# Performance work log

Measured on AMD Instinct MI355X. Metric: run time of the kernel, lower is better.

The kernel has to match this reference:

```python
import jax, jax.numpy as jnp
import numpy as np

N_TOK = 16384   # total tokens (batch*seq)
H = 2048        # hidden_size
I = 768         # moe_intermediate_size (per-expert MLP width)
TOPK = 8        # num_experts_per_tok


def setup_inputs() -> dict:
    key = jax.random.key(0)
    ks = jax.random.split(key, 7)
    hidden_states = jax.random.normal(ks[0], (N_TOK, H), dtype=jnp.float32)
    # expert_mask[j, k] != 0 means token k selected this expert at top-k slot j
    expert_mask = jax.random.randint(ks[1], (TOPK, N_TOK), 0, 2, dtype=jnp.int32)
    routing_weights = jax.random.uniform(ks[2], (N_TOK, TOPK), dtype=jnp.float32)
    final_hidden_states = jax.random.normal(ks[3], (N_TOK, H), dtype=jnp.float32)
    gate_w = jax.random.normal(ks[4], (I, H), dtype=jnp.float32) * 0.02
    up_w = jax.random.normal(ks[5], (I, H), dtype=jnp.float32) * 0.02
    down_w = jax.random.normal(ks[6], (H, I), dtype=jnp.float32) * 0.02
    return {
        "hidden_states": hidden_states,
        "expert_mask": expert_mask,
        "routing_weights": routing_weights,
        "final_hidden_states": final_hidden_states,
        "gate_w": gate_w,
        "up_w": up_w,
        "down_w": down_w,
    }


def reference(hidden_states, expert_mask, routing_weights, final_hidden_states,
              gate_w, up_w, down_w):
    # forward_expert: gather selected tokens, SwiGLU MLP, scale by routing weight,
    # scatter-add into final_hidden_states. Equivalent jit-friendly form: the
    # combined routing weight per token is w[k] = sum_j mask[j,k]*routing_weights[k,j]
    # (tokens selected multiple times are summed, matching index_add_ semantics),
    # and unselected tokens get w[k]=0 so they contribute nothing.
    g = hidden_states @ gate_w.T                       # [N, I]
    u = hidden_states @ up_w.T                         # [N, I]
    y = (jax.nn.silu(g) * u) @ down_w.T                # [N, H]
    w = jnp.einsum('jk,kj->k', expert_mask.astype(y.dtype), routing_weights)  # [N]
    return final_hidden_states + y * w[:, None]
```

## Files before the change

### kernel.cpp

```cpp
#include <hip/hip_runtime.h>
#include <stdint.h>

#define NTOK 16384
#define HD   2048
#define ID   768
#define TOPK 8

typedef __bf16 bf16x8 __attribute__((ext_vector_type(8)));
typedef float  floatx4 __attribute__((ext_vector_type(4)));
typedef unsigned short ushort8 __attribute__((ext_vector_type(8)));

__device__ __forceinline__ unsigned short f32_to_bf16_rne(float f) {
    union { float f; uint32_t u; } v; v.f = f;
    uint32_t u = v.u;
    u += 0x7FFFu + ((u >> 16) & 1u);
    return (unsigned short)(u >> 16);
}
__device__ __forceinline__ float bf16_to_f32(unsigned short h) {
    union { uint32_t u; float f; } v; v.u = ((uint32_t)h) << 16;
    return v.f;
}

#define GLD_LDS(gsrc, ldst)                                                              \
    __builtin_amdgcn_global_load_lds(                                                    \
        (const __attribute__((address_space(1))) uint32_t*)(const void*)(gsrc),          \
        (__attribute__((address_space(3))) uint32_t*)(void*)(ldst), 16, 0, 0)

template<int VM> __device__ __forceinline__ void wait_vm() {
    if constexpr (VM == 8)      asm volatile("s_waitcnt vmcnt(8)" ::: "memory");
    else if constexpr (VM == 3) asm volatile("s_waitcnt vmcnt(3)" ::: "memory");
    else if constexpr (VM == 2) asm volatile("s_waitcnt vmcnt(2)" ::: "memory");
    else                        asm volatile("s_waitcnt vmcnt(0)" ::: "memory");
}
#define BARRIER() do { asm volatile("" ::: "memory");              \
                       __builtin_amdgcn_s_barrier();               \
                       asm volatile("" ::: "memory"); } while (0)

__global__ __launch_bounds__(256) void compute_w_kernel(const int* __restrict__ mask,
                                                        const float* __restrict__ rw,
                                                        float* __restrict__ w) {
    int k = blockIdx.x * 256 + threadIdx.x;
    if (k >= NTOK) return;
    float acc = 0.f;
#pragma unroll
    for (int j = 0; j < TOPK; ++j)
        acc += (float)mask[j * NTOK + k] * rw[k * TOPK + j];
    w[k] = acc;
}

__global__ __launch_bounds__(256) void convert_hs_kernel(const float* __restrict__ src,
                                                         unsigned short* __restrict__ dst) {
    size_t i = (size_t)blockIdx.x * 256 + threadIdx.x;
    const float4* s = (const float4*)src;
    float4 a = s[2 * i], b = s[2 * i + 1];
    ushort8 o;
    o[0] = f32_to_bf16_rne(a.x); o[1] = f32_to_bf16_rne(a.y);
    o[2] = f32_to_bf16_rne(a.z); o[3] = f32_to_bf16_rne(a.w);
    o[4] = f32_to_bf16_rne(b.x); o[5] = f32_to_bf16_rne(b.y);
    o[6] = f32_to_bf16_rne(b.z); o[7] = f32_to_bf16_rne(b.w);
    *(ushort8*)(dst + 8 * i) = o;
}

__global__ __launch_bounds__(256) void convert_w3_kernel(const float* __restrict__ g,
                                                         const float* __restrict__ u,
                                                         const float* __restrict__ d,
                                                         unsigned short* __restrict__ dst) {
    int i = blockIdx.x * 256 + threadIdx.x;
    size_t e = (size_t)i * 8;
    const float* src;
    if (e < (size_t)2 * ID * HD) {
        int rd = (int)(e / HD);
        int c  = (int)(e - (size_t)rd * HD);
        int b = rd >> 4, h = (rd >> 3) & 1, sub = rd & 7;
        src = (h ? u : g) + (size_t)(b * 8 + sub) * HD + c;
    } else {
        src = d + (e - (size_t)2 * ID * HD);
    }
    const float4* s = (const float4*)src;
    float4 a = s[0], bq = s[1];
    ushort8 o;
    o[0] = f32_to_bf16_rne(a.x);  o[1] = f32_to_bf16_rne(a.y);
    o[2] = f32_to_bf16_rne(a.z);  o[3] = f32_to_bf16_rne(a.w);
    o[4] = f32_to_bf16_rne(bq.x); o[5] = f32_to_bf16_rne(bq.y);
    o[6] = f32_to_bf16_rne(bq.z); o[7] = f32_to_bf16_rne(bq.w);
    *(ushort8*)(dst + e) = o;
}

__global__ __launch_bounds__(512, 1) void gemm_gu_kernel(
    const unsigned short* __restrict__ A,
    const unsigned short* __restrict__ B,
    unsigned short* __restrict__ act) {
    constexpr int K = HD;
    constexpr int NT = K / 64;
    __shared__ __align__(16) unsigned char lds[2][57344];

    const int bid = blockIdx.x, nwg = gridDim.x;
    const int nb = (bid & 7) * (nwg >> 3) + (bid >> 3);
    const int bx = nb & 7, by = nb >> 3;
    const int row0 = by * 256, col0 = bx * 192;

    const int tid = threadIdx.x, wid = tid >> 6, lane = tid & 63;
    const int wr = wid >> 2, wc = wid & 3;
    const int lrow = lane & 15, q = lane >> 4;
    const int rsw = ((q ^ ((lrow >> 1) & 3)) << 4);

    const int kswz = (((lane & 3) ^ ((lane >> 3) & 3)) << 3);
    const unsigned short* sA[2];
#pragma unroll
    for (int h = 0; h < 2; ++h) {
        const int o = h * 8192 + wid * 1024 + lane * 16;
        sA[h] = A + (size_t)(row0 + (o >> 6)) * K + kswz;
    }
    const unsigned short* sB[3];
#pragma unroll
    for (int r = 0; r < 3; ++r) {
        const int o = r * 8192 + tid * 16;
        const int ks = (o >= 12288) ? 1 : 0;
        const int brow = (o - ks * 12288) >> 6;
        sB[r] = B + (size_t)(col0 + brow) * K + ks * 32 + kswz;
    }

#define STAGE_A(sb, ks, kt) do {                                                            \
        GLD_LDS(sA[0] + (kt) * 64 + (ks) * 32, lds[sb] + (ks) * 16384 + wid * 1024);        \
        GLD_LDS(sA[1] + (kt) * 64 + (ks) * 32, lds[sb] + (ks) * 16384 + 8192 + wid * 1024); \
    } while (0)
#define STAGE_B01(sb, kt) do {                                                              \
        GLD_LDS(sB[0] + (kt) * 64, lds[sb] + 32768 + wid * 1024);                           \
        GLD_LDS(sB[1] + (kt) * 64, lds[sb] + 32768 + 8192 + wid * 1024);                    \
    } while (0)
#define STAGE_B2(sb, kt)                                                                    \
        GLD_LDS(sB[2] + (kt) * 64, lds[sb] + 32768 + 16384 + wid * 1024)

#define READ_A4(dstv, sb, ks, mh) do { const unsigned char* rgn = lds[sb] + (ks) * 16384;   \
        _Pragma("unroll")                                                                   \
        for (int m = 0; m < 4; ++m)                                                         \
            dstv[m] = *(const bf16x8*)(rgn + (wr * 128 + ((mh) * 4 + m) * 16 + lrow) * 64 + rsw); \
    } while (0)
#define READ_B3(dstv, sb, ks) do { const unsigned char* rgn = lds[sb] + 32768 + (ks) * 12288; \
        _Pragma("unroll")                                                                   \
        for (int n = 0; n < 3; ++n)                                                         \
            dstv[n] = *(const bf16x8*)(rgn + (wc * 48 + n * 16 + lrow) * 64 + rsw);         \
    } while (0)
#define MFMA12(av, bv, mh) do {                                                             \
        __builtin_amdgcn_s_setprio(1);                                                      \
        _Pragma("unroll")                                                                   \
        for (int m = 0; m < 4; ++m)                                                         \
            _Pragma("unroll")                                                               \
            for (int n = 0; n < 3; ++n)                                                     \
                acc[(mh) * 4 + m][n] = __builtin_amdgcn_mfma_f32_16x16x32_bf16(av[m], bv[n], acc[(mh) * 4 + m][n], 0, 0, 0); \
        __builtin_amdgcn_s_setprio(0);                                                      \
    } while (0)

    floatx4 acc[8][3];
#pragma unroll
    for (int m = 0; m < 8; ++m)
#pragma unroll
        for (int n = 0; n < 3; ++n) acc[m][n] = (floatx4){0.f, 0.f, 0.f, 0.f};
    bf16x8 a03[4], a47[4], a03n[4], a47n[4], bb0[3], bb1[3];

    STAGE_A(0, 0, 0);
    STAGE_B01(0, 0);
    STAGE_A(0, 1, 0);
    STAGE_B2(0, 0);
    wait_vm<3>();
    BARRIER();
    READ_A4(a03, 0, 0, 0);
    READ_B3(bb0, 0, 0);

    for (int t = 0; t < NT - 1; ++t) {
        const int s = t & 1, sn = s ^ 1;
        STAGE_A(sn, 0, t + 1);
        MFMA12(a03, bb0, 0);
        READ_A4(a47, s, 0, 1);
        wait_vm<2>();
        BARRIER();
        STAGE_B01(sn, t + 1);
        MFMA12(a47, bb0, 1);
        READ_A4(a03n, s, 1, 0);
        READ_B3(bb1, s, 1);
        BARRIER();
        STAGE_A(sn, 1, t + 1);
        STAGE_B2(sn, t + 1);
        MFMA12(a03n, bb1, 0);
        READ_A4(a47n, s, 1, 1);
        wait_vm<3>();
        BARRIER();
        MFMA12(a47n, bb1, 1);
        READ_A4(a03, sn, 0, 0);
        READ_B3(bb0, sn, 0);
        BARRIER();
    }
    {
        const int s = (NT - 1) & 1;
        MFMA12(a03, bb0, 0);
        READ_A4(a47, s, 0, 1);
        wait_vm<0>();
        BARRIER();
        MFMA12(a47, bb0, 1);
        READ_A4(a03n, s, 1, 0);
        READ_B3(bb1, s, 1);
        BARRIER();
        MFMA12(a03n, bb1, 0);
        READ_A4(a47n, s, 1, 1);
        MFMA12(a47n, bb1, 1);
    }
#undef STAGE_A
#undef STAGE_B01
#undef STAGE_B2
#undef READ_A4
#undef READ_B3
#undef MFMA12

#pragma unroll
    for (int m = 0; m < 8; ++m) {
        const int rowb = row0 + wr * 128 + m * 16 + q * 4;
        float sv[3][4];
#pragma unroll
        for (int n = 0; n < 3; ++n)
#pragma unroll
            for (int r = 0; r < 4; ++r) {
                const float gf = acc[m][n][r];
                const float uf = __shfl_xor(gf, 8, 64);
                const float sig = __builtin_amdgcn_rcpf(1.f + __expf(-gf));
                sv[n][r] = gf * sig * uf;
            }
        if ((lrow & 8) == 0) {
            const int ib0 = (col0 >> 1) + wc * 24 + lrow;
#pragma unroll
            for (int n = 0; n < 3; ++n)
#pragma unroll
                for (int r = 0; r < 4; ++r)
                    act[(size_t)(rowb + r) * ID + ib0 + n * 8] = f32_to_bf16_rne(sv[n][r]);
        }
    }
}

__global__ __launch_bounds__(256, 2) void gemm_down_kernel(
    const unsigned short* __restrict__ A,
    const unsigned short* __restrict__ B,
    const float* __restrict__ fin,
    const float* __restrict__ wtok,
    float* __restrict__ out) {
    constexpr int K = ID;
    constexpr int NT = K / 64;
    __shared__ __align__(16) unsigned char lds[2][32768];

    const int bid = blockIdx.x, nwg = gridDim.x;
    const int nb = (bid & 7) * (nwg >> 3) + (bid >> 3);
    const int bx = nb & 15, by = nb >> 4;
    const int row0 = by * 128, col0 = bx * 128;

    const int tid = threadIdx.x, wid = tid >> 6, lane = tid & 63;
    const int wr = wid >> 1, wc = wid & 1;
    const int lrow = lane & 15, q = lane >> 4;

    const int srow = wid * 8 + (lane >> 3);
    const int sk = (((lane & 7) ^ ((lane >> 3) & 7)) << 3);
    const unsigned short* sA[4];
    const unsigned short* sB[4];
#pragma unroll
    for (int r = 0; r < 4; ++r) {
        sA[r] = A + (size_t)(row0 + r * 32 + srow) * K + sk;
        sB[r] = B + (size_t)(col0 + r * 32 + srow) * K + sk;
    }

#define STAGE_T(sb, kt) do {                                                    \
        _Pragma("unroll")                                                       \
        for (int r = 0; r < 4; ++r)                                             \
            GLD_LDS(sA[r] + (kt) * 64, lds[sb] + r * 4096 + wid * 1024);        \
        _Pragma("unroll")                                                       \
        for (int r = 0; r < 4; ++r)                                             \
            GLD_LDS(sB[r] + (kt) * 64, lds[sb] + 16384 + r * 4096 + wid * 1024);\
    } while (0)

    floatx4 acc[4][4];
#pragma unroll
    for (int m = 0; m < 4; ++m)
#pragma unroll
        for (int n = 0; n < 4; ++n) acc[m][n] = (floatx4){0.f, 0.f, 0.f, 0.f};
    bf16x8 af[4], bb[4];

    STAGE_T(0, 0);

    for (int t = 0; t < NT; ++t) {
        const int s = t & 1;
        if (t + 1 < NT) {
            STAGE_T(s ^ 1, t + 1);
            wait_vm<8>();
        } else {
            wait_vm<0>();
        }
        BARRIER();
        const unsigned char* la = lds[s];
        const unsigned char* lb = lds[s] + 16384;
#pragma unroll
        for (int ks = 0; ks < 2; ++ks) {
#pragma unroll
            for (int m = 0; m < 4; ++m)
                af[m] = *(const bf16x8*)(la + (wr * 64 + m * 16 + lrow) * 128 +
                                         (((ks * 4 + q) ^ (lrow & 7)) << 4));
#pragma unroll
            for (int n = 0; n < 4; ++n)
                bb[n] = *(const bf16x8*)(lb + (wc * 64 + n * 16 + lrow) * 128 +
                                         (((ks * 4 + q) ^ (lrow & 7)) << 4));
            __builtin_amdgcn_s_setprio(1);
#pragma unroll
            for (int m = 0; m < 4; ++m)
#pragma unroll
                for (int n = 0; n < 4; ++n)
                    acc[m][n] = __builtin_amdgcn_mfma_f32_16x16x32_bf16(af[m], bb[n], acc[m][n], 0, 0, 0);
            __builtin_amdgcn_s_setprio(0);
        }
        BARRIER();
    }
#undef STAGE_T

#pragma unroll
    for (int m = 0; m < 4; ++m)
#pragma unroll
        for (int r = 0; r < 4; ++r) {
            const int row = row0 + wr * 64 + m * 16 + q * 4 + r;
            const float wv = wtok[row];
#pragma unroll
            for (int n = 0; n < 4; ++n) {
                const int col = col0 + wc * 64 + n * 16 + lrow;
                out[(size_t)row * HD + col] = fin[(size_t)row * HD + col] + wv * acc[m][n][r];
            }
        }
}

extern "C" void kernel_launch(void* const* d_in, const int* in_sizes, int n_in,
                              void* d_out, int out_size, void* d_ws, size_t ws_size,
                              hipStream_t stream) {
    const float* hs   = (const float*)d_in[0];
    const int*   mask = (const int*)d_in[1];
    const float* rw   = (const float*)d_in[2];
    const float* fin  = (const float*)d_in[3];
    const float* gw   = (const float*)d_in[4];
    const float* uw   = (const float*)d_in[5];
    const float* dw   = (const float*)d_in[6];
    float* out = (float*)d_out;

    char* ws = (char*)d_ws;
    unsigned short* hs_b   = (unsigned short*)ws; ws += (size_t)NTOK * HD * 2;
    unsigned short* wcat_b = (unsigned short*)ws; ws += (size_t)3 * ID * HD * 2;
    unsigned short* act_b  = (unsigned short*)ws; ws += (size_t)NTOK * ID * 2;
    float* wtok = (float*)ws;
    unsigned short* down_b = wcat_b + (size_t)2 * ID * HD;

    compute_w_kernel<<<NTOK / 256, 256, 0, stream>>>(mask, rw, wtok);
    convert_hs_kernel<<<(NTOK * HD / 8) / 256, 256, 0, stream>>>(hs, hs_b);
    convert_w3_kernel<<<(3 * ID * HD / 8) / 256, 256, 0, stream>>>(gw, uw, dw, wcat_b);

    gemm_gu_kernel<<<512, 512, 0, stream>>>(hs_b, wcat_b, act_b);

    gemm_down_kernel<<<2048, 256, 0, stream>>>(act_b, down_b, fin, wtok, out);
}
```

Before: 224.9 us.

## Fuse fp32-to-bf16 hidden-state conversion into gate/up GEMM A-tile loading

Drops the separate hidden-state conversion kernel and bf16 workspace copy. The gate/up GEMM now loads fp32 A tiles into registers, converts them to bf16 and writes them swizzled into LDS, instead of DMA-ing bf16 tiles with global_load_lds. This removes a full 128MB-read/64MB-write pass and one launch. In exchange each block reads twice the A bytes (fp32), holds them in extra registers, and does conversion and LDS-write work inside the pipelined main loop, with retuned vmcnt waits.

Result: slower. 268.1 us (+19.2%).

```diff
diff --git a/kernel.cpp b/kernel.cpp
--- a/kernel.cpp
+++ b/kernel.cpp
@@ -9,6 +9,7 @@
 typedef __bf16 bf16x8 __attribute__((ext_vector_type(8)));
 typedef float  floatx4 __attribute__((ext_vector_type(4)));
 typedef unsigned short ushort8 __attribute__((ext_vector_type(8)));
+typedef unsigned short ushort4v __attribute__((ext_vector_type(4)));
 
 __device__ __forceinline__ unsigned short f32_to_bf16_rne(float f) {
     union { float f; uint32_t u; } v; v.f = f;
@@ -16,10 +17,6 @@
     u += 0x7FFFu + ((u >> 16) & 1u);
     return (unsigned short)(u >> 16);
 }
-__device__ __forceinline__ float bf16_to_f32(unsigned short h) {
-    union { uint32_t u; float f; } v; v.u = ((uint32_t)h) << 16;
-    return v.f;
-}
 
 #define GLD_LDS(gsrc, ldst)                                                              \
     __builtin_amdgcn_global_load_lds(                                                    \
@@ -27,11 +24,13 @@
         (__attribute__((address_space(3))) uint32_t*)(void*)(ldst), 16, 0, 0)
 
 template<int VM> __device__ __forceinline__ void wait_vm() {
-    if constexpr (VM == 8)      asm volatile("s_waitcnt vmcnt(8)" ::: "memory");
+    if constexpr (VM == 10)     asm volatile("s_waitcnt vmcnt(10)" ::: "memory");
+    else if constexpr (VM == 8) asm volatile("s_waitcnt vmcnt(8)" ::: "memory");
     else if constexpr (VM == 3) asm volatile("s_waitcnt vmcnt(3)" ::: "memory");
-    else if constexpr (VM == 2) asm volatile("s_waitcnt vmcnt(2)" ::: "memory");
+    else if constexpr (VM == 1) asm volatile("s_waitcnt vmcnt(1)" ::: "memory");
     else                        asm volatile("s_waitcnt vmcnt(0)" ::: "memory");
 }
+#define WAIT_LGKM0() asm volatile("s_waitcnt lgkmcnt(0)" ::: "memory")
 #define BARRIER() do { asm volatile("" ::: "memory");              \
                        __builtin_amdgcn_s_barrier();               \
                        asm volatile("" ::: "memory"); } while (0)
@@ -46,19 +45,6 @@
     for (int j = 0; j < TOPK; ++j)
         acc += (float)mask[j * NTOK + k] * rw[k * TOPK + j];
     w[k] = acc;
-}
-
-__global__ __launch_bounds__(256) void convert_hs_kernel(const float* __restrict__ src,
-                                                         unsigned short* __restrict__ dst) {
-    size_t i = (size_t)blockIdx.x * 256 + threadIdx.x;
-    const float4* s = (const float4*)src;
-    float4 a = s[2 * i], b = s[2 * i + 1];
-    ushort8 o;
-    o[0] = f32_to_bf16_rne(a.x); o[1] = f32_to_bf16_rne(a.y);
-    o[2] = f32_to_bf16_rne(a.z); o[3] = f32_to_bf16_rne(a.w);
-    o[4] = f32_to_bf16_rne(b.x); o[5] = f32_to_bf16_rne(b.y);
-    o[6] = f32_to_bf16_rne(b.z); o[7] = f32_to_bf16_rne(b.w);
-    *(ushort8*)(dst + 8 * i) = o;
 }
 
 __global__ __launch_bounds__(256) void convert_w3_kernel(const float* __restrict__ g,
@@ -87,7 +73,7 @@
 }
 
 __global__ __launch_bounds__(512, 1) void gemm_gu_kernel(
-    const unsigned short* __restrict__ A,
+    const float* __restrict__ A,
     const unsigned short* __restrict__ B,
     unsigned short* __restrict__ act) {
     constexpr int K = HD;
@@ -104,13 +90,20 @@
     const int lrow = lane & 15, q = lane >> 4;
     const int rsw = ((q ^ ((lrow >> 1) & 3)) << 4);
 
+    const int rbase = wid * 32 + (lane >> 4);
+    const float* sAreg = A + (size_t)(row0 + rbase) * K + (lane & 15) * 4;
+    const int a_ks = (lane >> 3) & 1;
+    const int a_c  = (lane >> 1) & 3;
+    const int a_half = (lane & 1) * 8;
+    int a_waddr[8];
+#pragma unroll
+    for (int i = 0; i < 8; ++i) {
+        const int rL = rbase + i * 4;
+        const int key = (rL >> 1) & 3;
+        a_waddr[i] = a_ks * 16384 + rL * 64 + ((a_c ^ key) << 4) + a_half;
+    }
+
     const int kswz = (((lane & 3) ^ ((lane >> 3) & 3)) << 3);
-    const unsigned short* sA[2];
-#pragma unroll
-    for (int h = 0; h < 2; ++h) {
-        const int o = h * 8192 + wid * 1024 + lane * 16;
-        sA[h] = A + (size_t)(row0 + (o >> 6)) * K + kswz;
-    }
     const unsigned short* sB[3];
 #pragma unroll
     for (int r = 0; r < 3; ++r) {
@@ -120,9 +113,21 @@
         sB[r] = B + (size_t)(col0 + brow) * K + ks * 32 + kswz;
     }
 
-#define STAGE_A(sb, ks, kt) do {                                                            \
-        GLD_LDS(sA[0] + (kt) * 64 + (ks) * 32, lds[sb] + (ks) * 16384 + wid * 1024);        \
-        GLD_LDS(sA[1] + (kt) * 64 + (ks) * 32, lds[sb] + (ks) * 16384 + 8192 + wid * 1024); \
+#define ISSUE_A(kt) do {                                                                    \
+        _Pragma("unroll")                                                                   \
+        for (int i = 0; i < 8; ++i)                                                         \
+            av[i] = *(const floatx4*)(sAreg + (size_t)i * 4 * K + (size_t)(kt) * 64);       \
+    } while (0)
+#define CVT_WRITE(sb) do {                                                                  \
+        _Pragma("unroll")                                                                   \
+        for (int i = 0; i < 8; ++i) {                                                       \
+            ushort4v pk;                                                                    \
+            pk[0] = __builtin_bit_cast(unsigned short, (__bf16)av[i][0]);                   \
+            pk[1] = __builtin_bit_cast(unsigned short, (__bf16)av[i][1]);                   \
+            pk[2] = __builtin_bit_cast(unsigned short, (__bf16)av[i][2]);                   \
+            pk[3] = __builtin_bit_cast(unsigned short, (__bf16)av[i][3]);                   \
+            *(ushort4v*)(lds[sb] + a_waddr[i]) = pk;                                        \
+        }                                                                                   \
     } while (0)
 #define STAGE_B01(sb, kt) do {                                                              \
         GLD_LDS(sB[0] + (kt) * 64, lds[sb] + 32768 + wid * 1024);                           \
@@ -141,13 +146,13 @@
         for (int n = 0; n < 3; ++n)                                                         \
             dstv[n] = *(const bf16x8*)(rgn + (wc * 48 + n * 16 + lrow) * 64 + rsw);         \
     } while (0)
-#define MFMA12(av, bv, mh) do {                                                             \
+#define MFMA12(avv, bv, mh) do {                                                            \
         __builtin_amdgcn_s_setprio(1);                                                      \
         _Pragma("unroll")                                                                   \
         for (int m = 0; m < 4; ++m)                                                         \
             _Pragma("unroll")                                                               \
             for (int n = 0; n < 3; ++n)                                                     \
-                acc[(mh) * 4 + m][n] = __builtin_amdgcn_mfma_f32_16x16x32_bf16(av[m], bv[n], acc[(mh) * 4 + m][n], 0, 0, 0); \
+                acc[(mh) * 4 + m][n] = __builtin_amdgcn_mfma_f32_16x16x32_bf16(avv[m], bv[n], acc[(mh) * 4 + m][n], 0, 0, 0); \
         __builtin_amdgcn_s_setprio(0);                                                      \
     } while (0)
 
@@ -157,33 +162,37 @@
 #pragma unroll
         for (int n = 0; n < 3; ++n) acc[m][n] = (floatx4){0.f, 0.f, 0.f, 0.f};
     bf16x8 a03[4], a47[4], a03n[4], a47n[4], bb0[3], bb1[3];
-
-    STAGE_A(0, 0, 0);
+    floatx4 av[8];
+
+    ISSUE_A(0);
     STAGE_B01(0, 0);
-    STAGE_A(0, 1, 0);
     STAGE_B2(0, 0);
     wait_vm<3>();
+    CVT_WRITE(0);
+    wait_vm<1>();
+    WAIT_LGKM0();
     BARRIER();
     READ_A4(a03, 0, 0, 0);
     READ_B3(bb0, 0, 0);
 
     for (int t = 0; t < NT - 1; ++t) {
         const int s = t & 1, sn = s ^ 1;
-        STAGE_A(sn, 0, t + 1);
+        STAGE_B01(sn, t + 1);
+        ISSUE_A(t + 1);
         MFMA12(a03, bb0, 0);
         READ_A4(a47, s, 0, 1);
-        wait_vm<2>();
-        BARRIER();
-        STAGE_B01(sn, t + 1);
+        wait_vm<10>();
+        BARRIER();
+        STAGE_B2(sn, t + 1);
         MFMA12(a47, bb0, 1);
         READ_A4(a03n, s, 1, 0);
         READ_B3(bb1, s, 1);
         BARRIER();
-        STAGE_A(sn, 1, t + 1);
-        STAGE_B2(sn, t + 1);
         MFMA12(a03n, bb1, 0);
         READ_A4(a47n, s, 1, 1);
-        wait_vm<3>();
+        wait_vm<1>();
+        CVT_WRITE(sn);
+        WAIT_LGKM0();
         BARRIER();
         MFMA12(a47n, bb1, 1);
         READ_A4(a03, sn, 0, 0);
@@ -204,7 +213,8 @@
         READ_A4(a47n, s, 1, 1);
         MFMA12(a47n, bb1, 1);
     }
-#undef STAGE_A
+#undef ISSUE_A
+#undef CVT_WRITE
 #undef STAGE_B01
 #undef STAGE_B2
 #undef READ_A4
@@ -342,17 +352,15 @@
     float* out = (float*)d_out;
 
     char* ws = (char*)d_ws;
-    unsigned short* hs_b   = (unsigned short*)ws; ws += (size_t)NTOK * HD * 2;
     unsigned short* wcat_b = (unsigned short*)ws; ws += (size_t)3 * ID * HD * 2;
     unsigned short* act_b  = (unsigned short*)ws; ws += (size_t)NTOK * ID * 2;
     float* wtok = (float*)ws;
     unsigned short* down_b = wcat_b + (size_t)2 * ID * HD;
 
     compute_w_kernel<<<NTOK / 256, 256, 0, stream>>>(mask, rw, wtok);
-    convert_hs_kernel<<<(NTOK * HD / 8) / 256, 256, 0, stream>>>(hs, hs_b);
     convert_w3_kernel<<<(3 * ID * HD / 8) / 256, 256, 0, stream>>>(gw, uw, dw, wcat_b);
 
-    gemm_gu_kernel<<<512, 512, 0, stream>>>(hs_b, wcat_b, act_b);
+    gemm_gu_kernel<<<512, 512, 0, stream>>>(hs, wcat_b, act_b);
 
     gemm_down_kernel<<<2048, 256, 0, stream>>>(act_b, down_b, fin, wtok, out);
 }
```
